# Optimization experiments

Measured on AMD Instinct MI355X. Metric: run time of the kernel, lower is better.

## Reference

```python
import jax, jax.numpy as jnp
import numpy as np

N, E = 100000, 1600000
DIM, H, D = 64, 4, 8          # dim, num_heads, qk_dim
DH = D * H                    # 32
QK_SCALE = (DIM // H) ** -0.5


def setup_inputs() -> dict:
    key = jax.random.key(0)
    k1, k2, k3, k4 = jax.random.split(key, 4)
    x = jax.random.normal(k1, (N, DIM), dtype=jnp.float32)
    edge_index = jax.random.randint(k2, (2, E), 0, N, dtype=jnp.int64)
    W_qkv = jax.random.normal(k3, (DIM, 2 * DH + DIM), dtype=jnp.float32) * (DIM ** -0.5)
    b_qkv = jax.random.normal(k4, (2 * DH + DIM,), dtype=jnp.float32) * 0.02
    return {"x": x, "edge_index": edge_index, "W_qkv": W_qkv, "b_qkv": b_qkv}


def reference(x, edge_index, W_qkv, b_qkv):
    n = x.shape[0]
    e = edge_index.shape[1]
    qkv = x @ W_qkv + b_qkv                       # (N, 2*DH+DIM)
    q = qkv[:, :DH].reshape(n, H, D)
    k = qkv[:, DH:2 * DH].reshape(n, H, D)
    v = qkv[:, 2 * DH:].reshape(n, H, DIM // H)
    s, t = edge_index[0], edge_index[1]
    q_e = q[s] * QK_SCALE                         # (E, H, D)
    k_e = k[t]
    v_e = v[t]                                    # (E, H, DIM/H)
    # scale q by 1/sqrt(num source neighbors) (bincount of s)
    deg = jax.ops.segment_sum(jnp.ones((e,), x.dtype), s, num_segments=n)
    q_e = q_e * (deg[s] ** -0.5)[:, None, None]
    compat = jnp.einsum('ehd,ehd->eh', q_e, k_e)  # (E, H)
    # segment softmax over edges grouped by source node s
    m = jax.ops.segment_max(compat, s, num_segments=n)
    ex = jnp.exp(compat - m[s])
    denom = jax.ops.segment_sum(ex, s, num_segments=n)
    attn = ex / (denom[s] + 1e-16)                # (E, H)
    msg = (v_e * attn[..., None]).reshape(e, DIM)  # (E, DIM)
    out = jax.ops.segment_sum(msg, s, num_segments=n)  # (N, DIM)
    return out
```

## Files before the change

kernel.cpp:

```cpp
#include <hip/hip_runtime.h>


#define NDIM 64
#define NBMAX 1024
#define CTILE 8192
#define STGMAX 4352

static __device__ __forceinline__ unsigned short f2bf(float f) {
    unsigned int u = __float_as_uint(f);
    unsigned int r = (u + 0x7fffu + ((u >> 16) & 1u)) >> 16;
    return (unsigned short)r;
}

__global__ void bucket_count_kernel(const int* __restrict__ s_arr,
                                    unsigned int* __restrict__ bcnt, int E) {
    __shared__ unsigned int h[NBMAX];
    for (int i = threadIdx.x; i < NBMAX; i += blockDim.x) h[i] = 0;
    __syncthreads();
    int i0 = blockIdx.x * blockDim.x + threadIdx.x;
    int st = gridDim.x * blockDim.x;
    for (int e = i0; e < E; e += st)
        atomicAdd(&h[(unsigned)s_arr[e] >> 7], 1u);
    __syncthreads();
    for (int i = threadIdx.x; i < NBMAX; i += blockDim.x)
        if (h[i]) atomicAdd(&bcnt[i], h[i]);
}

__global__ void scan_buckets_kernel(const unsigned int* __restrict__ bcnt,
                                    unsigned int* __restrict__ bbase,
                                    unsigned int* __restrict__ gcur) {
    __shared__ unsigned int sh[1024];
    int tid = threadIdx.x;
    unsigned int v = bcnt[tid];
    unsigned int acc = v;
    sh[tid] = acc;
    __syncthreads();
    for (int off = 1; off < 1024; off <<= 1) {
        unsigned int add = (tid >= off) ? sh[tid - off] : 0;
        __syncthreads();
        acc += add;
        sh[tid] = acc;
        __syncthreads();
    }
    bbase[tid] = acc - v;
    gcur[tid]  = acc - v;
}

__global__ void __launch_bounds__(1024, 2)
bin_kernel(const int* __restrict__ s_arr,
           const int* __restrict__ t_arr,
           unsigned int* __restrict__ gcur,
           unsigned int* __restrict__ binned, int E) {
    __shared__ unsigned int hist[NBMAX];
    __shared__ unsigned int off[NBMAX];
    __shared__ unsigned int gbase[NBMAX];
    __shared__ unsigned int stg[CTILE];
    __shared__ unsigned int psum[NBMAX];
    int tid = threadIdx.x;
    int e0 = blockIdx.x * CTILE;
    int cnt = min(CTILE, E - e0);

    hist[tid] = 0;
    __syncthreads();
    for (int i = tid; i < cnt; i += 1024)
        atomicAdd(&hist[(unsigned)s_arr[e0 + i] >> 7], 1u);
    __syncthreads();

    unsigned int v = hist[tid];
    unsigned int acc = v;
    psum[tid] = acc;
    __syncthreads();
    for (int o = 1; o < 1024; o <<= 1) {
        unsigned int add = (tid >= o) ? psum[tid - o] : 0;
        __syncthreads();
        acc += add;
        psum[tid] = acc;
        __syncthreads();
    }
    off[tid] = acc - v;
    __syncthreads();

    for (int i = tid; i < cnt; i += 1024) {
        int s = s_arr[e0 + i];
        int t = t_arr[e0 + i];
        unsigned int bkt = (unsigned)s >> 7;
        unsigned int p = atomicAdd(&off[bkt], 1u);
        stg[p] = ((unsigned)(s & 127) << 17) | (unsigned)t;
    }
    __syncthreads();

    {
        unsigned int h = hist[tid];
        gbase[tid] = h ? atomicAdd(&gcur[tid], h) : 0u;
    }
    __syncthreads();

    int wid = tid >> 6, lane = tid & 63;
    for (int b = wid; b < NBMAX; b += 16) {
        unsigned int h = hist[b];
        if (h == 0) continue;
        unsigned int src = off[b] - h;
        unsigned int dst = gbase[b];
        for (unsigned int i = lane; i < h; i += 64)
            binned[dst + i] = stg[src + i];
    }
}

__global__ void qkv_gemm_kernel(const float* __restrict__ x,
                                const float* __restrict__ W,
                                const float* __restrict__ b,
                                float* __restrict__ qs,
                                unsigned short* __restrict__ kv, int N) {
    int col = threadIdx.x & 127;
    int rw  = threadIdx.x >> 7;
    float w[64];
    #pragma unroll
    for (int k = 0; k < 64; ++k) w[k] = W[k * 128 + col];
    float bias = b[col];
    __shared__ float4 xs[8][16];

    for (int r0 = blockIdx.x * 8; r0 < N; r0 += gridDim.x * 8) {
        __syncthreads();
        if (threadIdx.x < 128) {
            int rr = threadIdx.x >> 4;
            int cc = threadIdx.x & 15;
            int n = r0 + rr;
            xs[rr][cc] = (n < N)
                ? reinterpret_cast<const float4*>(x)[(size_t)n * 16 + cc]
                : make_float4(0.f, 0.f, 0.f, 0.f);
        }
        __syncthreads();
        #pragma unroll
        for (int rsub = 0; rsub < 4; ++rsub) {
            int rr = rw * 4 + rsub;
            int n = r0 + rr;
            if (n < N) {
                float acc = bias;
                #pragma unroll
                for (int k4 = 0; k4 < 16; ++k4) {
                    float4 xv = xs[rr][k4];
                    acc = fmaf(xv.x, w[4 * k4 + 0], acc);
                    acc = fmaf(xv.y, w[4 * k4 + 1], acc);
                    acc = fmaf(xv.z, w[4 * k4 + 2], acc);
                    acc = fmaf(xv.w, w[4 * k4 + 3], acc);
                }
                if (col < 32) {
                    qs[(size_t)n * 32 + col] = acc;
                } else if (col < 64) {
                    kv[(size_t)n * 96 + (col - 32)] = f2bf(acc);
                } else {
                    kv[(size_t)n * 96 + 32 + (col - 64)] = f2bf(acc);
                }
            }
        }
    }
}

#define COMPUTE_EDGE(rr)                                              \
    {                                                                 \
        float lo = __uint_as_float((rr) << 16);                       \
        float hi = __uint_as_float((rr) & 0xffff0000u);               \
        float p = fmaf(q0, lo, q1 * hi);                              \
        p += __shfl_xor(p, 1);                                        \
        p += __shfl_xor(p, 2);                                        \
        float c = __shfl(p, csrc);                                    \
        float w = __expf(c);                                          \
        accx = fmaf(w, lo, accx);                                     \
        accy = fmaf(w, hi, accy);                                     \
        den += w;                                                     \
    }

__global__ void __launch_bounds__(512, 8)
sort_aggregate_kernel(const unsigned int* __restrict__ bbase,
                      const unsigned int* __restrict__ bcnt,
                      const unsigned int* __restrict__ binned,
                      const float* __restrict__ qs,
                      const unsigned int* __restrict__ kv32,
                      float* __restrict__ out, int N) {
    __shared__ unsigned int hist[128];
    __shared__ unsigned int rstart[128];
    __shared__ unsigned int cur[128];
    __shared__ unsigned int sh[128];
    __shared__ unsigned int stg[STGMAX];

    int b = blockIdx.x;
    int tid = threadIdx.x;
    unsigned int base = bbase[b];
    unsigned int cnt = min(bcnt[b], (unsigned int)STGMAX);

    if (tid < 128) hist[tid] = 0;
    __syncthreads();
    for (unsigned int i = tid; i < cnt; i += 512)
        atomicAdd(&hist[binned[base + i] >> 17], 1u);
    __syncthreads();

    unsigned int v = (tid < 128) ? hist[tid] : 0;
    unsigned int acc = v;
    if (tid < 128) sh[tid] = acc;
    __syncthreads();
    for (int o = 1; o < 128; o <<= 1) {
        unsigned int add = (tid >= o && tid < 128) ? sh[tid - o] : 0;
        __syncthreads();
        if (tid < 128) { acc += add; sh[tid] = acc; }
        __syncthreads();
    }
    if (tid < 128) {
        unsigned int exc = acc - v;
        rstart[tid] = exc;
        cur[tid] = exc;
    }
    __syncthreads();

    for (unsigned int i = tid; i < cnt; i += 512) {
        unsigned int e = binned[base + i];
        unsigned int p = atomicAdd(&cur[e >> 17], 1u);
        stg[p] = (e & 0x1FFFFu) * 192u;
    }
    __syncthreads();

    int wid = tid >> 6, lane = tid & 63;
    unsigned int lane4 = ((unsigned int)lane) << 2;
    bool ldact = (lane < 48);
    const char* kvb = (const char*)kv32;
    int csrc = (lane < 16) ? (lane & ~3)
             : (lane < 48) ? (((lane - 16) >> 3) << 2)
                           : 0;

    for (int nl = wid * 16; nl < wid * 16 + 16; ++nl) {
        int n = b * 128 + nl;
        if (n >= N) break;
        int dg = (int)hist[nl];
        if (dg == 0) {
            if (lane >= 16 && lane < 48)
                *reinterpret_cast<float2*>(&out[(size_t)n * 64 + 2 * (lane - 16)]) =
                    make_float2(0.f, 0.f);
            continue;
        }
        int start = (int)rstart[nl];
        float sc = 0.25f * rsqrtf((float)dg);
        float q0 = 0.f, q1 = 0.f;
        if (lane < 16) {
            q0 = qs[(size_t)n * 32 + 2 * lane] * sc;
            q1 = qs[(size_t)n * 32 + 2 * lane + 1] * sc;
        }

        float accx = 0.f, accy = 0.f, den = 0.f;
        int j = start;
        int rem = dg;

        unsigned int ra0 = 0, ra1 = 0, ra2 = 0, ra3 = 0;
        if (rem >= 4) {
            unsigned int o0 = stg[j] + lane4,     o1 = stg[j + 1] + lane4;
            unsigned int o2 = stg[j + 2] + lane4, o3 = stg[j + 3] + lane4;
            if (ldact) {
                ra0 = *(const unsigned int*)(kvb + o0);
                ra1 = *(const unsigned int*)(kvb + o1);
                ra2 = *(const unsigned int*)(kvb + o2);
                ra3 = *(const unsigned int*)(kvb + o3);
            }
        }
        while (rem >= 4) {
            unsigned int rb0 = 0, rb1 = 0, rb2 = 0, rb3 = 0;
            if (rem >= 8) {
                unsigned int o0 = stg[j + 4] + lane4, o1 = stg[j + 5] + lane4;
                unsigned int o2 = stg[j + 6] + lane4, o3 = stg[j + 7] + lane4;
                if (ldact) {
                    rb0 = *(const unsigned int*)(kvb + o0);
                    rb1 = *(const unsigned int*)(kvb + o1);
                    rb2 = *(const unsigned int*)(kvb + o2);
                    rb3 = *(const unsigned int*)(kvb + o3);
                }
            }
            COMPUTE_EDGE(ra0);
            COMPUTE_EDGE(ra1);
            COMPUTE_EDGE(ra2);
            COMPUTE_EDGE(ra3);
            ra0 = rb0; ra1 = rb1; ra2 = rb2; ra3 = rb3;
            j += 4; rem -= 4;
        }
        for (; rem > 0; --rem, ++j) {
            unsigned int o0 = stg[j] + lane4;
            unsigned int r0 = ldact ? *(const unsigned int*)(kvb + o0) : 0u;
            COMPUTE_EDGE(r0);
        }

        if (lane >= 16 && lane < 48) {
            float inv = 1.0f / (den + 1e-16f);
            float2 o = make_float2(accx * inv, accy * inv);
            *reinterpret_cast<float2*>(&out[(size_t)n * 64 + 2 * (lane - 16)]) = o;
        }
    }
}

extern "C" void kernel_launch(void* const* d_in, const int* in_sizes, int n_in,
                              void* d_out, int out_size, void* d_ws, size_t ws_size,
                              hipStream_t stream) {
    const float* x = (const float*)d_in[0];
    const int*   eidx = (const int*)d_in[1];
    const float* W = (const float*)d_in[2];
    const float* b = (const float*)d_in[3];
    int N = in_sizes[0] / NDIM;
    int E = in_sizes[1] / 2;
    float* out = (float*)d_out;

    int NB = (N + 127) / 128;

    float* qs = (float*)d_ws;
    unsigned short* kv = (unsigned short*)(qs + (size_t)N * 32);
    unsigned int* bcnt  = (unsigned int*)(kv + (size_t)N * 96);
    unsigned int* bbase = bcnt + NBMAX;
    unsigned int* gcur  = bbase + NBMAX;
    unsigned int* binned = gcur + NBMAX;

    const int* s_arr = eidx;
    const int* t_arr = eidx + E;

    hipMemsetAsync(bcnt, 0, NBMAX * sizeof(unsigned int), stream);

    bucket_count_kernel<<<512, 256, 0, stream>>>(s_arr, bcnt, E);
    scan_buckets_kernel<<<1, 1024, 0, stream>>>(bcnt, bbase, gcur);
    bin_kernel<<<(E + CTILE - 1) / CTILE, 1024, 0, stream>>>(s_arr, t_arr, gcur, binned, E);
    qkv_gemm_kernel<<<2048, 256, 0, stream>>>(x, W, b, qs, kv, N);
    sort_aggregate_kernel<<<NB, 512, 0, stream>>>(
        bbase, bcnt, binned, qs, (const unsigned int*)kv, out, N);
}
```

Before: 178.3 us.

## Fuse QKV GEMM with bucket count, shrink bin tiles, stage binned edges in LDS

The QKV projection and the per-bucket edge count now run as one launch, with some blocks doing the GEMM and the rest doing the histogram. This removes a kernel launch and lets the two independent phases share the GPU. The bin kernel moves to 512 threads with 4096-edge tiles and a two-entries-per-thread scan, aiming for more resident blocks. The aggregate kernel copies its bucket of binned edges into LDS once instead of reading global memory twice, which costs extra LDS and may lower occupancy.

```diff
diff --git a/kernel.cpp b/kernel.cpp
--- a/kernel.cpp
+++ b/kernel.cpp
@@ -3,8 +3,10 @@
 
 #define NDIM 64
 #define NBMAX 1024
-#define CTILE 8192
+#define CTILE 4096
 #define STGMAX 4352
+#define GEMM_BLKS 1536
+#define CNT_BLKS 512
 
 static __device__ __forceinline__ unsigned short f2bf(float f) {
     unsigned int u = __float_as_uint(f);
@@ -12,18 +14,68 @@
     return (unsigned short)r;
 }
 
-__global__ void bucket_count_kernel(const int* __restrict__ s_arr,
-                                    unsigned int* __restrict__ bcnt, int E) {
-    __shared__ unsigned int h[NBMAX];
-    for (int i = threadIdx.x; i < NBMAX; i += blockDim.x) h[i] = 0;
-    __syncthreads();
-    int i0 = blockIdx.x * blockDim.x + threadIdx.x;
-    int st = gridDim.x * blockDim.x;
-    for (int e = i0; e < E; e += st)
-        atomicAdd(&h[(unsigned)s_arr[e] >> 7], 1u);
-    __syncthreads();
-    for (int i = threadIdx.x; i < NBMAX; i += blockDim.x)
-        if (h[i]) atomicAdd(&bcnt[i], h[i]);
+__global__ void fused_gemm_count_kernel(const float* __restrict__ x,
+                                        const float* __restrict__ W,
+                                        const float* __restrict__ bvec,
+                                        float* __restrict__ qs,
+                                        unsigned short* __restrict__ kv,
+                                        const int* __restrict__ s_arr,
+                                        unsigned int* __restrict__ bcnt,
+                                        int N, int E) {
+    __shared__ unsigned int sm[1024];
+    if (blockIdx.x < GEMM_BLKS) {
+        float4* xs = (float4*)sm;
+        int col = threadIdx.x & 127;
+        int rw  = threadIdx.x >> 7;
+        float w[64];
+        #pragma unroll
+        for (int k = 0; k < 64; ++k) w[k] = W[k * 128 + col];
+        float bias = bvec[col];
+        for (int r0 = blockIdx.x * 8; r0 < N; r0 += GEMM_BLKS * 8) {
+            __syncthreads();
+            if (threadIdx.x < 128) {
+                int rr = threadIdx.x >> 4;
+                int cc = threadIdx.x & 15;
+                int n = r0 + rr;
+                xs[rr * 16 + cc] = (n < N)
+                    ? reinterpret_cast<const float4*>(x)[(size_t)n * 16 + cc]
+                    : make_float4(0.f, 0.f, 0.f, 0.f);
+            }
+            __syncthreads();
+            #pragma unroll
+            for (int rsub = 0; rsub < 4; ++rsub) {
+                int rr = rw * 4 + rsub;
+                int n = r0 + rr;
+                if (n < N) {
+                    float acc = bias;
+                    #pragma unroll
+                    for (int k4 = 0; k4 < 16; ++k4) {
+                        float4 xv = xs[rr * 16 + k4];
+                        acc = fmaf(xv.x, w[4 * k4 + 0], acc);
+                        acc = fmaf(xv.y, w[4 * k4 + 1], acc);
+                        acc = fmaf(xv.z, w[4 * k4 + 2], acc);
+                        acc = fmaf(xv.w, w[4 * k4 + 3], acc);
+                    }
+                    if (col < 32) {
+                        qs[(size_t)n * 32 + col] = acc;
+                    } else if (col < 64) {
+                        kv[(size_t)n * 96 + (col - 32)] = f2bf(acc);
+                    } else {
+                        kv[(size_t)n * 96 + 32 + (col - 64)] = f2bf(acc);
+                    }
+                }
+            }
+        }
+    } else {
+        int bid = blockIdx.x - GEMM_BLKS;
+        for (int i = threadIdx.x; i < NBMAX; i += 256) sm[i] = 0;
+        __syncthreads();
+        for (int e = bid * 256 + threadIdx.x; e < E; e += CNT_BLKS * 256)
+            atomicAdd(&sm[(unsigned)s_arr[e] >> 7], 1u);
+        __syncthreads();
+        for (int i = threadIdx.x; i < NBMAX; i += 256)
+            if (sm[i]) atomicAdd(&bcnt[i], sm[i]);
+    }
 }
 
 __global__ void scan_buckets_kernel(const unsigned int* __restrict__ bcnt,
@@ -46,41 +98,44 @@
     gcur[tid]  = acc - v;
 }
 
-__global__ void __launch_bounds__(1024, 2)
-bin_kernel(const int* __restrict__ s_arr,
-           const int* __restrict__ t_arr,
-           unsigned int* __restrict__ gcur,
-           unsigned int* __restrict__ binned, int E) {
+__global__ void bin_kernel(const int* __restrict__ s_arr,
+                           const int* __restrict__ t_arr,
+                           unsigned int* __restrict__ gcur,
+                           unsigned int* __restrict__ binned, int E) {
     __shared__ unsigned int hist[NBMAX];
     __shared__ unsigned int off[NBMAX];
     __shared__ unsigned int gbase[NBMAX];
     __shared__ unsigned int stg[CTILE];
-    __shared__ unsigned int psum[NBMAX];
+    __shared__ unsigned int psum[512];
     int tid = threadIdx.x;
     int e0 = blockIdx.x * CTILE;
     int cnt = min(CTILE, E - e0);
 
-    hist[tid] = 0;
-    __syncthreads();
-    for (int i = tid; i < cnt; i += 1024)
+    for (int i = tid; i < NBMAX; i += 512) hist[i] = 0;
+    __syncthreads();
+    for (int i = tid; i < cnt; i += 512)
         atomicAdd(&hist[(unsigned)s_arr[e0 + i] >> 7], 1u);
     __syncthreads();
 
-    unsigned int v = hist[tid];
-    unsigned int acc = v;
+    unsigned int a0 = hist[2 * tid];
+    unsigned int a1 = hist[2 * tid + 1];
+    unsigned int ps = a0 + a1;
+    unsigned int acc = ps;
     psum[tid] = acc;
     __syncthreads();
-    for (int o = 1; o < 1024; o <<= 1) {
+    for (int o = 1; o < 512; o <<= 1) {
         unsigned int add = (tid >= o) ? psum[tid - o] : 0;
         __syncthreads();
         acc += add;
         psum[tid] = acc;
         __syncthreads();
     }
-    off[tid] = acc - v;
-    __syncthreads();
-
-    for (int i = tid; i < cnt; i += 1024) {
+    unsigned int exc = acc - ps;
+    off[2 * tid]     = exc;
+    off[2 * tid + 1] = exc + a0;
+    __syncthreads();
+
+    for (int i = tid; i < cnt; i += 512) {
         int s = s_arr[e0 + i];
         int t = t_arr[e0 + i];
         unsigned int bkt = (unsigned)s >> 7;
@@ -89,70 +144,20 @@
     }
     __syncthreads();
 
-    {
-        unsigned int h = hist[tid];
-        gbase[tid] = h ? atomicAdd(&gcur[tid], h) : 0u;
+    for (int i = tid; i < NBMAX; i += 512) {
+        unsigned int h = hist[i];
+        gbase[i] = h ? atomicAdd(&gcur[i], h) : 0u;
     }
     __syncthreads();
 
     int wid = tid >> 6, lane = tid & 63;
-    for (int b = wid; b < NBMAX; b += 16) {
+    for (int b = wid; b < NBMAX; b += 8) {
         unsigned int h = hist[b];
         if (h == 0) continue;
         unsigned int src = off[b] - h;
         unsigned int dst = gbase[b];
         for (unsigned int i = lane; i < h; i += 64)
             binned[dst + i] = stg[src + i];
-    }
-}
-
-__global__ void qkv_gemm_kernel(const float* __restrict__ x,
-                                const float* __restrict__ W,
-                                const float* __restrict__ b,
-                                float* __restrict__ qs,
-                                unsigned short* __restrict__ kv, int N) {
-    int col = threadIdx.x & 127;
-    int rw  = threadIdx.x >> 7;
-    float w[64];
-    #pragma unroll
-    for (int k = 0; k < 64; ++k) w[k] = W[k * 128 + col];
-    float bias = b[col];
-    __shared__ float4 xs[8][16];
-
-    for (int r0 = blockIdx.x * 8; r0 < N; r0 += gridDim.x * 8) {
-        __syncthreads();
-        if (threadIdx.x < 128) {
-            int rr = threadIdx.x >> 4;
-            int cc = threadIdx.x & 15;
-            int n = r0 + rr;
-            xs[rr][cc] = (n < N)
-                ? reinterpret_cast<const float4*>(x)[(size_t)n * 16 + cc]
-                : make_float4(0.f, 0.f, 0.f, 0.f);
-        }
-        __syncthreads();
-        #pragma unroll
-        for (int rsub = 0; rsub < 4; ++rsub) {
-            int rr = rw * 4 + rsub;
-            int n = r0 + rr;
-            if (n < N) {
-                float acc = bias;
-                #pragma unroll
-                for (int k4 = 0; k4 < 16; ++k4) {
-                    float4 xv = xs[rr][k4];
-                    acc = fmaf(xv.x, w[4 * k4 + 0], acc);
-                    acc = fmaf(xv.y, w[4 * k4 + 1], acc);
-                    acc = fmaf(xv.z, w[4 * k4 + 2], acc);
-                    acc = fmaf(xv.w, w[4 * k4 + 3], acc);
-                }
-                if (col < 32) {
-                    qs[(size_t)n * 32 + col] = acc;
-                } else if (col < 64) {
-                    kv[(size_t)n * 96 + (col - 32)] = f2bf(acc);
-                } else {
-                    kv[(size_t)n * 96 + 32 + (col - 64)] = f2bf(acc);
-                }
-            }
-        }
     }
 }
 
@@ -181,6 +186,7 @@
     __shared__ unsigned int rstart[128];
     __shared__ unsigned int cur[128];
     __shared__ unsigned int sh[128];
+    __shared__ unsigned int raw[STGMAX];
     __shared__ unsigned int stg[STGMAX];
 
     int b = blockIdx.x;
@@ -191,7 +197,10 @@
     if (tid < 128) hist[tid] = 0;
     __syncthreads();
     for (unsigned int i = tid; i < cnt; i += 512)
-        atomicAdd(&hist[binned[base + i] >> 17], 1u);
+        raw[i] = binned[base + i];
+    __syncthreads();
+    for (unsigned int i = tid; i < cnt; i += 512)
+        atomicAdd(&hist[raw[i] >> 17], 1u);
     __syncthreads();
 
     unsigned int v = (tid < 128) ? hist[tid] : 0;
@@ -212,7 +221,7 @@
     __syncthreads();
 
     for (unsigned int i = tid; i < cnt; i += 512) {
-        unsigned int e = binned[base + i];
+        unsigned int e = raw[i];
         unsigned int p = atomicAdd(&cur[e >> 17], 1u);
         stg[p] = (e & 0x1FFFFu) * 192u;
     }
@@ -317,10 +326,10 @@
 
     hipMemsetAsync(bcnt, 0, NBMAX * sizeof(unsigned int), stream);
 
-    bucket_count_kernel<<<512, 256, 0, stream>>>(s_arr, bcnt, E);
+    fused_gemm_count_kernel<<<GEMM_BLKS + CNT_BLKS, 256, 0, stream>>>(
+        x, W, b, qs, kv, s_arr, bcnt, N, E);
     scan_buckets_kernel<<<1, 1024, 0, stream>>>(bcnt, bbase, gcur);
-    bin_kernel<<<(E + CTILE - 1) / CTILE, 1024, 0, stream>>>(s_arr, t_arr, gcur, binned, E);
-    qkv_gemm_kernel<<<2048, 256, 0, stream>>>(x, W, b, qs, kv, N);
+    bin_kernel<<<(E + CTILE - 1) / CTILE, 512, 0, stream>>>(s_arr, t_arr, gcur, binned, E);
     sort_aggregate_kernel<<<NB, 512, 0, stream>>>(
         bbase, bcnt, binned, qs, (const unsigned int*)kv, out, N);
 }
```

After: 188.2 us. +5.6%, slower.
